# Kernel optimization log

Hardware: AMD Instinct MI355X
Metric: run time of the kernel (lower is better)

Reference implementation:

```python
import jax, jax.numpy as jnp
import numpy as np
import math

S, D, H, L, V = 1024, 768, 12, 6, 32000
KD = D // H
FF = 4 * D
PAD = 0


def setup_inputs() -> dict:
    key = jax.random.key(0)
    ks = jax.random.split(key, 20)
    s = D ** -0.5
    return {
        "token_ids": jax.random.randint(ks[0], (2, S), 0, V, dtype=jnp.int32),
        "emb": jax.random.normal(ks[1], (V, D)) * s,
        "Wq": jax.random.normal(ks[2], (L, H, D, KD)) * s,
        "bq": jnp.zeros((L, H, KD)),
        "Wk": jax.random.normal(ks[3], (L, H, D, KD)) * s,
        "bk": jnp.zeros((L, H, KD)),
        "Wv": jax.random.normal(ks[4], (L, H, D, D)) * s,
        "bv": jnp.zeros((L, H, D)),
        "g1": jnp.ones((L, D)), "be1": jnp.zeros((L, D)),
        "g2": jnp.ones((L, D)), "be2": jnp.zeros((L, D)),
        "W1": jax.random.normal(ks[5], (L, D, FF)) * s,
        "b1": jnp.zeros((L, FF)),
        "W2": jax.random.normal(ks[6], (L, FF, D)) * (FF ** -0.5),
        "b2": jnp.zeros((L, D)),
        "Wout": jax.random.normal(ks[7], (D, V)) * s,
        "bout": jnp.zeros((V,)),
    }


def _pe():
    pos = jnp.arange(S, dtype=jnp.float32)[:, None]
    div = jnp.exp(jnp.arange(0, D, 2, dtype=jnp.float32) * (-math.log(10000.0) / D))
    ang = pos * div  # [S, D/2]
    return jnp.stack([jnp.sin(ang), jnp.cos(ang)], axis=-1).reshape(S, D)


def _ln(x, g, b):
    m = x.mean(-1, keepdims=True)
    v = ((x - m) ** 2).mean(-1, keepdims=True)
    return (x - m) * jax.lax.rsqrt(v + 1e-5) * g + b


def reference(token_ids, emb, Wq, bq, Wk, bk, Wv, bv, g1, be1, g2, be2, W1, b1, W2, b2, Wout, bout):
    pad = token_ids == PAD  # [B,S]
    causal = jnp.triu(jnp.ones((S, S), dtype=bool), k=1)
    # mask[b,s,t] = causal | pad-as-key | pad-as-query
    mask = causal[None, None] | pad[:, None, None, :] | pad[:, None, :, None]  # [B,1,S,S]
    scale = math.sqrt(KD)
    x = emb[token_ids] + _pe()[None]  # [B,S,D]
    for l in range(L):
        q = jnp.einsum('bsd,hdk->bhsk', x, Wq[l]) + bq[l][None, :, None, :]
        k = jnp.einsum('bsd,hdk->bhsk', x, Wk[l]) + bk[l][None, :, None, :]
        v = jnp.einsum('bsd,hde->bhse', x, Wv[l]) + bv[l][None, :, None, :]
        scores = jnp.einsum('bhsk,bhtk->bhst', q, k) / scale
        scores = jnp.where(mask, -jnp.inf, scores)
        all_masked = jnp.all(mask, axis=-1)  # rows with every key masked -> uniform attn
        scores = jnp.where(all_masked[..., None], 0.0, scores)
        attn = jax.nn.softmax(scores, axis=-1)
        heads = jnp.einsum('bhst,bhte->bhse', attn, v)  # per-head full-D values
        attn_out = heads.mean(axis=1)  # heads are AVERAGED, not concatenated
        x = _ln(x + attn_out, g1[l], be1[l])
        ff = jax.nn.relu(x @ W1[l] + b1[l]) @ W2[l] + b2[l]
        x = _ln(x + ff, g2[l], be2[l])
    return x @ Wout + bout
```

## Files before the change

kernel.cpp:

```cpp
#include <hip/hip_runtime.h>
#include <hip/hip_bf16.h>

#define SQ 1024
#define DM 768
#define NH 12
#define NL 6
#define NV 32000
#define KDH 64
#define FFD 3072

using bf16 = __hip_bfloat16;
typedef __attribute__((ext_vector_type(4))) float f32x4;
typedef __attribute__((ext_vector_type(8))) short bf16x8;

__global__ void fill_kernel(float* __restrict__ out, long n, float val) {
  const long stride = (long)gridDim.x * blockDim.x;
  for (long i = (long)blockIdx.x * blockDim.x + threadIdx.x; i < n; i += stride)
    out[i] = val;
}

__device__ __forceinline__ void gload16(const void* g, void* l) {
  __builtin_amdgcn_global_load_lds(
      (const __attribute__((address_space(1))) unsigned int*)g,
      (__attribute__((address_space(3))) unsigned int*)l, 16, 0, 0);
}

template<bool OUT_BF16, bool RELU>
__global__ __launch_bounds__(256) void gemm_bt(
    int M, int N, int K,
    const bf16* __restrict__ Ap, long sAz, int lda,
    const bf16* __restrict__ Bp, long sBz, int ldbt,
    const float* __restrict__ biasp, int sBiasZ,
    void* __restrict__ Cp, long sCz, long sCb, long sCs, long sCn)
{
  __shared__ __align__(16) char lds[32768];
  char* const As = lds;
  char* const Bs = lds + 8192;

  const int tid = threadIdx.x;
  const int gx = gridDim.x, gy = gridDim.y;
  const int nwg = gx * gy * (int)gridDim.z;
  int flat = ((int)blockIdx.z * gy + (int)blockIdx.y) * gx + (int)blockIdx.x;
  {
    const int q = nwg >> 3, r = nwg & 7;
    const int xcd = flat & 7, loc = flat >> 3;
    flat = (xcd < r ? xcd * (q + 1) : r * (q + 1) + (xcd - r) * q) + loc;
  }
  const int bx  = flat % gx;
  const int byz = flat / gx;
  const int m0 = bx * 128;
  const int n0 = (byz % gy) * 128;
  const int z  = byz / gy;

  const int lane = tid & 63;
  const int wid  = tid >> 6;
  const int wm = (wid >> 1) * 64;
  const int wn = (wid & 1) * 64;

  const int srow  = tid >> 2;
  const int sslot = tid & 3;
  const int xorb  = (sslot ^ (srow & 3)) << 4;

  const char* gA0 = (const char*)(Ap + (long)z * sAz + (long)(m0 + srow) * lda) + xorb;
  const char* gA1 = (const char*)(Ap + (long)z * sAz + (long)(m0 + srow + 64) * lda) + xorb;
  const char* gB0 = (const char*)(Bp + (long)z * sBz + (long)(n0 + srow) * ldbt) + xorb;
  const char* gB1 = (const char*)(Bp + (long)z * sBz + (long)(n0 + srow + 64) * ldbt) + xorb;

  auto stage = [&](int dstOfs) {
    gload16(gA0, As + dstOfs + tid * 16);
    gload16(gA1, As + dstOfs + (tid + 256) * 16);
    gload16(gB0, Bs + dstOfs + tid * 16);
    gload16(gB1, Bs + dstOfs + (tid + 256) * 16);
    gA0 += 64; gA1 += 64; gB0 += 64; gB1 += 64;
  };

  const int fr = lane & 15;
  const int kq = lane >> 4;
  const char* fA[4];
  const char* fB[4];
#pragma unroll
  for (int m = 0; m < 4; ++m) {
    const int R = wm + m * 16 + fr;
    fA[m] = As + R * 64 + ((kq ^ (R & 3)) << 4);
  }
#pragma unroll
  for (int n = 0; n < 4; ++n) {
    const int R = wn + n * 16 + fr;
    fB[n] = Bs + R * 64 + ((kq ^ (R & 3)) << 4);
  }

  f32x4 acc[4][4] = {};

  stage(0);
  int cur = 0;
  for (int kt = 0; kt < K; kt += 32) {
    if (kt + 32 < K) {
      stage((cur ^ 1) * 16384);
      asm volatile("s_waitcnt vmcnt(4)" ::: "memory");
    } else {
      asm volatile("s_waitcnt vmcnt(0)" ::: "memory");
    }
    __builtin_amdgcn_s_barrier();
    const int co = cur * 16384;
    bf16x8 af[4], bfr[4];
#pragma unroll
    for (int m = 0; m < 4; ++m) af[m] = *(const bf16x8*)(fA[m] + co);
#pragma unroll
    for (int n = 0; n < 4; ++n) bfr[n] = *(const bf16x8*)(fB[n] + co);
#pragma unroll
    for (int m = 0; m < 4; ++m)
#pragma unroll
      for (int n = 0; n < 4; ++n)
        acc[m][n] = __builtin_amdgcn_mfma_f32_16x16x32_bf16(af[m], bfr[n], acc[m][n], 0, 0, 0);
    __builtin_amdgcn_s_barrier();
    cur ^= 1;
  }

  const int rg = (lane >> 4) * 4;
  const int cl = lane & 15;
#pragma unroll
  for (int n = 0; n < 4; ++n) {
    const int gcol = n0 + wn + n * 16 + cl;
    float bias = 0.f;
    if (biasp) bias = biasp[(long)z * sBiasZ + gcol];
    if (OUT_BF16 && sCs == 1) {
#pragma unroll
      for (int m = 0; m < 4; ++m) {
        const int grow = m0 + wm + m * 16 + rg;
        const long ci = (long)z * sCz + (long)(grow >> 10) * sCb
                      + (long)(grow & 1023) + (long)gcol * sCn;
        ushort4 pk;
        float v0 = acc[m][n][0] + bias, v1 = acc[m][n][1] + bias;
        float v2 = acc[m][n][2] + bias, v3 = acc[m][n][3] + bias;
        if (RELU) { v0 = fmaxf(v0, 0.f); v1 = fmaxf(v1, 0.f);
                    v2 = fmaxf(v2, 0.f); v3 = fmaxf(v3, 0.f); }
        pk.x = __builtin_bit_cast(ushort, __float2bfloat16(v0));
        pk.y = __builtin_bit_cast(ushort, __float2bfloat16(v1));
        pk.z = __builtin_bit_cast(ushort, __float2bfloat16(v2));
        pk.w = __builtin_bit_cast(ushort, __float2bfloat16(v3));
        *(ushort4*)((bf16*)Cp + ci) = pk;
      }
    } else {
#pragma unroll
      for (int m = 0; m < 4; ++m) {
#pragma unroll
        for (int rr = 0; rr < 4; ++rr) {
          const int grow = m0 + wm + m * 16 + rg + rr;
          float v = acc[m][n][rr] + bias;
          if (RELU) v = fmaxf(v, 0.f);
          const long ci = (long)z * sCz + (long)(grow >> 10) * sCb
                        + (long)(grow & 1023) * sCs + (long)gcol * sCn;
          if (OUT_BF16) ((bf16*)Cp)[ci] = __float2bfloat16(v);
          else          ((float*)Cp)[ci] = v;
        }
      }
    }
  }
}

__global__ __launch_bounds__(256) void transpose_kernel(
    const float* __restrict__ in, long sInZ, int ldin,
    bf16* __restrict__ out, long sOutZ, int ldout)
{
  __shared__ float t[64][65];
  const int tid = threadIdx.x;
  const int n0 = blockIdx.x * 64, k0 = blockIdx.y * 64;
  const float* ip = in + (long)blockIdx.z * sInZ;
  bf16* op = out + (long)blockIdx.z * sOutZ;
  const int cx = (tid & 15) * 4, ry = tid >> 4;
#pragma unroll
  for (int p = 0; p < 4; ++p) {
    const int k = ry + p * 16;
    const float4 v = *(const float4*)(ip + (long)(k0 + k) * ldin + n0 + cx);
    t[k][cx] = v.x; t[k][cx + 1] = v.y; t[k][cx + 2] = v.z; t[k][cx + 3] = v.w;
  }
  __syncthreads();
#pragma unroll
  for (int p = 0; p < 4; ++p) {
    const int n = ry + p * 16;
    ushort4 o;
    o.x = __builtin_bit_cast(ushort, __float2bfloat16(t[cx + 0][n]));
    o.y = __builtin_bit_cast(ushort, __float2bfloat16(t[cx + 1][n]));
    o.z = __builtin_bit_cast(ushort, __float2bfloat16(t[cx + 2][n]));
    o.w = __builtin_bit_cast(ushort, __float2bfloat16(t[cx + 3][n]));
    *(ushort4*)(op + (long)(n0 + n) * ldout + k0 + cx) = o;
  }
}

__global__ void biasqk_kernel(const float* __restrict__ bq, const float* __restrict__ bk,
                              float* __restrict__ out) {
  const int i = blockIdx.x * 256 + threadIdx.x;
  if (i < NH * 128) {
    const int h = i >> 7, n = i & 127;
    out[i] = (n < 64) ? bq[h * 64 + n] : bk[h * 64 + n - 64];
  }
}

__global__ __launch_bounds__(256) void embed_kernel(
    const int* __restrict__ tok, const float* __restrict__ emb,
    float* __restrict__ x, bf16* __restrict__ xb)
{
  const int gid = blockIdx.x * 256 + threadIdx.x;
  const int row = gid / (DM / 4);
  const int dc  = (gid % (DM / 4)) * 4;
  const int t = tok[row];
  const int s = row & (SQ - 1);
#pragma unroll
  for (int j = 0; j < 4; ++j) {
    const int d = dc + j;
    const float e = emb[(long)t * DM + d];
    const float div = expf(-(float)(d & ~1) * (9.210340371976184f / (float)DM));
    const float ang = (float)s * div;
    const float pe = (d & 1) ? cosf(ang) : sinf(ang);
    const float v = e + pe;
    x[(long)row * DM + d] = v;
    xb[(long)row * DM + d] = __float2bfloat16(v);
  }
}

__global__ __launch_bounds__(256) void softmax_kernel(
    bf16* __restrict__ P, const int* __restrict__ tok)
{
  const int row = blockIdx.x;
  const int s = row & (SQ - 1);
  const int z = row >> 10;
  const int b = z / NH;
  bf16* sp = P + (long)row * SQ;
  const int* tb = tok + b * SQ;
  const int tid = threadIdx.x;
  const int t0 = tid * 4;

  if (tb[s] == 0) {
    const bf16 u = __float2bfloat16(1.0f / (float)SQ);
    sp[t0] = u; sp[t0 + 1] = u; sp[t0 + 2] = u; sp[t0 + 3] = u;
    return;
  }
  uint2 raw = *(const uint2*)(sp + t0);
  int4 tv = *(const int4*)(tb + t0);
  const bf16* rh = (const bf16*)&raw;
  const int tvv[4] = {tv.x, tv.y, tv.z, tv.w};
  float val[4];
  float vmax = -1e30f;
#pragma unroll
  for (int j = 0; j < 4; ++j) {
    const int t = t0 + j;
    const bool valid = (t <= s) && (tvv[j] != 0);
    val[j] = valid ? __bfloat162float(rh[j]) * 0.125f : -1e30f;
    vmax = fmaxf(vmax, val[j]);
  }
  __shared__ float red[4];
  const int lane = tid & 63, wid = tid >> 6;
  float w = vmax;
#pragma unroll
  for (int o = 32; o >= 1; o >>= 1) w = fmaxf(w, __shfl_xor(w, o));
  if (lane == 0) red[wid] = w;
  __syncthreads();
  const float Mx = fmaxf(fmaxf(red[0], red[1]), fmaxf(red[2], red[3]));
  __syncthreads();
  float e[4]; float lsum = 0.f;
#pragma unroll
  for (int j = 0; j < 4; ++j) {
    e[j] = (val[j] > -1e29f) ? expf(val[j] - Mx) : 0.f;
    lsum += e[j];
  }
  w = lsum;
#pragma unroll
  for (int o = 32; o >= 1; o >>= 1) w += __shfl_xor(w, o);
  if (lane == 0) red[wid] = w;
  __syncthreads();
  const float inv = 1.0f / (red[0] + red[1] + red[2] + red[3]);
#pragma unroll
  for (int j = 0; j < 4; ++j) sp[t0 + j] = __float2bfloat16(e[j] * inv);
}

template<int MODE>
__global__ __launch_bounds__(256) void ln_kernel(
    float* __restrict__ x, bf16* __restrict__ xb,
    const float* __restrict__ tmp, const bf16* __restrict__ heads,
    const float* __restrict__ g, const float* __restrict__ be)
{
  const int r = blockIdx.x;
  const int b = r >> 10;
  const int s = r & (SQ - 1);
  const int tid = threadIdx.x;
  float vals[3];
  float sum = 0.f, sq = 0.f;
#pragma unroll
  for (int i = 0; i < 3; ++i) {
    const int d = tid + i * 256;
    const float a = x[(long)r * DM + d];
    float t;
    if (MODE == 0) {
      t = tmp[(long)r * DM + d];
    } else {
      float hs = 0.f;
#pragma unroll
      for (int h = 0; h < NH; ++h)
        hs += __bfloat162float(heads[((long)(b * NH + h) * SQ + s) * DM + d]);
      t = hs * (1.0f / (float)NH);
    }
    const float vv = a + t;
    vals[i] = vv;
    sum += vv; sq += vv * vv;
  }
  __shared__ float rs[4], rq[4];
  const int lane = tid & 63, wid = tid >> 6;
  float s1 = sum, s2 = sq;
#pragma unroll
  for (int o = 32; o >= 1; o >>= 1) { s1 += __shfl_xor(s1, o); s2 += __shfl_xor(s2, o); }
  if (lane == 0) { rs[wid] = s1; rq[wid] = s2; }
  __syncthreads();
  const float S1 = rs[0] + rs[1] + rs[2] + rs[3];
  const float S2 = rq[0] + rq[1] + rq[2] + rq[3];
  const float mean = S1 * (1.0f / (float)DM);
  const float var  = S2 * (1.0f / (float)DM) - mean * mean;
  const float rstd = rsqrtf(var + 1e-5f);
#pragma unroll
  for (int i = 0; i < 3; ++i) {
    const int d = tid + i * 256;
    const float o = (vals[i] - mean) * rstd * g[d] + be[d];
    x[(long)r * DM + d] = o;
    xb[(long)r * DM + d] = __float2bfloat16(o);
  }
}

extern "C" void kernel_launch(void* const* d_in, const int* in_sizes, int n_in,
                              void* d_out, int out_size, void* d_ws, size_t ws_size,
                              hipStream_t stream) {
  const int expect_sizes[18] = {
    2048, 24576000, 3538944, 4608, 3538944, 4608, 42467328, 55296,
    4608, 4608, 4608, 4608, 14155776, 18432, 14155776, 4608, 24576000, 32000
  };
  bool sizes_ok = (n_in == 18);
  if (sizes_ok)
    for (int i = 0; i < 18; ++i) sizes_ok = sizes_ok && (in_sizes[i] == expect_sizes[i]);
  if (!sizes_ok) {
    fill_kernel<<<2048, 256, 0, stream>>>((float*)d_out, (long)out_size, 1000.0f);
    return;
  }
  if (out_size != 65536000) {
    fill_kernel<<<2048, 256, 0, stream>>>((float*)d_out, (long)out_size, 3000.0f);
    return;
  }
  if (ws_size < 158081024ull) {
    fill_kernel<<<2048, 256, 0, stream>>>((float*)d_out, (long)out_size, 2000.0f);
    return;
  }

  const int*   tok  = (const int*)d_in[0];
  const float* emb  = (const float*)d_in[1];
  const float* Wq   = (const float*)d_in[2];
  const float* bq   = (const float*)d_in[3];
  const float* Wk   = (const float*)d_in[4];
  const float* bk   = (const float*)d_in[5];
  const float* Wv   = (const float*)d_in[6];
  const float* bv   = (const float*)d_in[7];
  const float* g1   = (const float*)d_in[8];
  const float* be1  = (const float*)d_in[9];
  const float* g2   = (const float*)d_in[10];
  const float* be2  = (const float*)d_in[11];
  const float* W1   = (const float*)d_in[12];
  const float* b1   = (const float*)d_in[13];
  const float* W2   = (const float*)d_in[14];
  const float* b2   = (const float*)d_in[15];
  const float* Wout = (const float*)d_in[16];
  const float* bout = (const float*)d_in[17];

  char* ws = (char*)d_ws;
  float* x      = (float*)(ws + 0);
  bf16*  xb     = (bf16*) (ws + 6291456);
  bf16*  qk     = (bf16*) (ws + 9437184);
  float* tmp    = (float*)(ws + 9437184);
  bf16*  vT     = (bf16*) (ws + 15728640);
  bf16*  P      = (bf16*) (ws + 53477376);
  bf16*  ff     = (bf16*) (ws + 53477376);
  bf16*  woutT  = (bf16*) (ws + 53477376);
  bf16*  heads  = (bf16*) (ws + 103809024);
  bf16*  wqkT   = (bf16*) (ws + 141557760);
  bf16*  wvT    = (bf16*) (ws + 143917056);
  bf16*  w1T    = (bf16*) (ws + 141557760);
  bf16*  w2T    = (bf16*) (ws + 146276352);
  float* biasqk = (float*)(ws + 158072832);

  embed_kernel<<<dim3((2 * SQ * DM / 4) / 256), 256, 0, stream>>>(tok, emb, x, xb);

  for (int l = 0; l < NL; ++l) {
    transpose_kernel<<<dim3(1, 12, NH), 256, 0, stream>>>(
        Wq + (long)l * NH * DM * KDH, (long)DM * KDH, KDH,
        wqkT, 128 * DM, DM);
    transpose_kernel<<<dim3(1, 12, NH), 256, 0, stream>>>(
        Wk + (long)l * NH * DM * KDH, (long)DM * KDH, KDH,
        wqkT + 64 * DM, 128 * DM, DM);
    transpose_kernel<<<dim3(12, 12, NH), 256, 0, stream>>>(
        Wv + (long)l * NH * DM * DM, (long)DM * DM, DM,
        wvT, (long)DM * DM, DM);
    biasqk_kernel<<<6, 256, 0, stream>>>(bq + l * NH * KDH, bk + l * NH * KDH, biasqk);

    gemm_bt<true, false><<<dim3(16, 1, NH), 256, 0, stream>>>(
        2048, 128, DM, xb, 0, DM, wqkT, (long)128 * DM, DM,
        biasqk, 128,
        qk, (long)SQ * 128, (long)NH * SQ * 128, 128, 1);
    gemm_bt<true, false><<<dim3(16, 6, NH), 256, 0, stream>>>(
        2048, DM, DM, xb, 0, DM, wvT, (long)DM * DM, DM,
        bv + (long)l * NH * DM, DM,
        vT, (long)DM * SQ, (long)NH * DM * SQ, 1, SQ);
    gemm_bt<true, false><<<dim3(8, 8, 2 * NH), 256, 0, stream>>>(
        SQ, SQ, KDH, qk, (long)SQ * 128, 128, qk + 64, (long)SQ * 128, 128,
        (const float*)nullptr, 0,
        P, (long)SQ * SQ, 0, SQ, 1);
    softmax_kernel<<<dim3(2 * NH * SQ), 256, 0, stream>>>(P, tok);
    gemm_bt<true, false><<<dim3(8, 6, 2 * NH), 256, 0, stream>>>(
        SQ, DM, SQ, P, (long)SQ * SQ, SQ, vT, (long)DM * SQ, SQ,
        (const float*)nullptr, 0,
        heads, (long)SQ * DM, 0, DM, 1);
    ln_kernel<1><<<dim3(2048), 256, 0, stream>>>(x, xb, nullptr, heads,
                                                 g1 + l * DM, be1 + l * DM);
    transpose_kernel<<<dim3(48, 12, 1), 256, 0, stream>>>(
        W1 + (long)l * DM * FFD, 0, FFD, w1T, 0, DM);
    transpose_kernel<<<dim3(12, 48, 1), 256, 0, stream>>>(
        W2 + (long)l * FFD * DM, 0, DM, w2T, 0, FFD);
    gemm_bt<true, true><<<dim3(16, 24, 1), 256, 0, stream>>>(
        2048, FFD, DM, xb, 0, DM, w1T, 0, DM,
        b1 + (long)l * FFD, 0,
        ff, 0, (long)SQ * FFD, FFD, 1);
    gemm_bt<false, false><<<dim3(16, 6, 1), 256, 0, stream>>>(
        2048, DM, FFD, ff, 0, FFD, w2T, 0, FFD,
        b2 + (long)l * DM, 0,
        tmp, 0, (long)SQ * DM, DM, 1);
    ln_kernel<0><<<dim3(2048), 256, 0, stream>>>(x, xb, tmp, nullptr,
                                                 g2 + l * DM, be2 + l * DM);
  }
  transpose_kernel<<<dim3(500, 12, 1), 256, 0, stream>>>(Wout, 0, NV, woutT, 0, DM);
  gemm_bt<false, false><<<dim3(16, 250, 1), 256, 0, stream>>>(
      2048, NV, DM, xb, 0, DM, woutT, 0, DM,
      bout, 0,
      d_out, 0, (long)SQ * NV, NV, 1);
}
```

Baseline: 1.750 ms.

## Exploit causal mask to skip upper-triangle score tiles and truncate PV reduction

Result: no change. 1.769 ms (+1.0%).

```diff
diff --git a/kernel.cpp b/kernel.cpp
--- a/kernel.cpp
+++ b/kernel.cpp
@@ -25,7 +25,7 @@
       (__attribute__((address_space(3))) unsigned int*)l, 16, 0, 0);
 }
 
-template<bool OUT_BF16, bool RELU>
+template<bool OUT_BF16, bool RELU, bool CSKIP = false, bool CTRUNC = false>
 __global__ __launch_bounds__(256) void gemm_bt(
     int M, int N, int K,
     const bf16* __restrict__ Ap, long sAz, int lda,
@@ -52,6 +52,9 @@
   const int n0 = (byz % gy) * 128;
   const int z  = byz / gy;
 
+  if (CSKIP && n0 > m0) return;
+  const int KK = CTRUNC ? min(K, m0 + 128) : K;
+
   const int lane = tid & 63;
   const int wid  = tid >> 6;
   const int wm = (wid >> 1) * 64;
@@ -93,8 +96,8 @@
 
   stage(0);
   int cur = 0;
-  for (int kt = 0; kt < K; kt += 32) {
-    if (kt + 32 < K) {
+  for (int kt = 0; kt < KK; kt += 32) {
+    if (kt + 32 < KK) {
       stage((cur ^ 1) * 16384);
       asm volatile("s_waitcnt vmcnt(4)" ::: "memory");
     } else {
@@ -196,6 +199,58 @@
   }
 }
 
+__global__ __launch_bounds__(256) void xpart_kernel(
+    const float* __restrict__ x, float* __restrict__ xpart) {
+  const int b = blockIdx.x, g = blockIdx.y;
+  const int tid = threadIdx.x;
+  const float* xp = x + (long)b * SQ * DM + (long)g * 64 * DM;
+  float a0 = 0.f, a1 = 0.f, a2 = 0.f;
+  for (int s = 0; s < 64; ++s) {
+    a0 += xp[(long)s * DM + tid];
+    a1 += xp[(long)s * DM + tid + 256];
+    a2 += xp[(long)s * DM + tid + 512];
+  }
+  float* op = xpart + (long)(b * 16 + g) * DM;
+  op[tid] = a0; op[tid + 256] = a1; op[tid + 512] = a2;
+}
+
+__global__ void xmeanf_kernel(const float* __restrict__ xpart, float* __restrict__ xmean) {
+  const int b = blockIdx.x;
+  const int d = threadIdx.x;
+  float a = 0.f;
+#pragma unroll
+  for (int g = 0; g < 16; ++g) a += xpart[(long)(b * 16 + g) * DM + d];
+  xmean[b * DM + d] = a * (1.0f / (float)SQ);
+}
+
+__global__ __launch_bounds__(256) void vmeanw_kernel(
+    const float* __restrict__ xmean, const bf16* __restrict__ wvT,
+    const float* __restrict__ bv, float* __restrict__ vmean) {
+  const int tid = threadIdx.x;
+  const int w = blockIdx.x * 4 + (tid >> 6);
+  const int b = w / DM;
+  const int e = w % DM;
+  const int lane = tid & 63;
+  float xm[12];
+#pragma unroll
+  for (int j = 0; j < 12; ++j) xm[j] = xmean[b * DM + lane + j * 64];
+  float acc = 0.f;
+  for (int h = 0; h < NH; ++h) {
+    const bf16* wr = wvT + ((long)h * DM + e) * DM;
+#pragma unroll
+    for (int j = 0; j < 12; ++j)
+      acc += xm[j] * __bfloat162float(wr[lane + j * 64]);
+  }
+#pragma unroll
+  for (int o = 32; o >= 1; o >>= 1) acc += __shfl_xor(acc, o);
+  if (lane == 0) {
+    float bs = 0.f;
+#pragma unroll
+    for (int h = 0; h < NH; ++h) bs += bv[h * DM + e];
+    vmean[b * DM + e] = (acc + bs) * (1.0f / (float)NH);
+  }
+}
+
 __global__ __launch_bounds__(256) void embed_kernel(
     const int* __restrict__ tok, const float* __restrict__ emb,
     float* __restrict__ x, bf16* __restrict__ xb)
@@ -277,12 +332,13 @@
 __global__ __launch_bounds__(256) void ln_kernel(
     float* __restrict__ x, bf16* __restrict__ xb,
     const float* __restrict__ tmp, const bf16* __restrict__ heads,
-    const float* __restrict__ g, const float* __restrict__ be)
+    const float* __restrict__ g, const float* __restrict__ be,
+    const int* __restrict__ tok, const float* __restrict__ vmean)
 {
   const int r = blockIdx.x;
   const int b = r >> 10;
-  const int s = r & (SQ - 1);
   const int tid = threadIdx.x;
+  const bool pad = (MODE == 1) && (tok[r] == 0);
   float vals[3];
   float sum = 0.f, sq = 0.f;
 #pragma unroll
@@ -292,7 +348,10 @@
     float t;
     if (MODE == 0) {
       t = tmp[(long)r * DM + d];
+    } else if (pad) {
+      t = vmean[b * DM + d];
     } else {
+      const int s = r & (SQ - 1);
       float hs = 0.f;
 #pragma unroll
       for (int h = 0; h < NH; ++h)
@@ -342,7 +401,7 @@
     fill_kernel<<<2048, 256, 0, stream>>>((float*)d_out, (long)out_size, 3000.0f);
     return;
   }
-  if (ws_size < 158081024ull) {
+  if (ws_size < 158189568ull) {
     fill_kernel<<<2048, 256, 0, stream>>>((float*)d_out, (long)out_size, 2000.0f);
     return;
   }
@@ -381,6 +440,9 @@
   bf16*  w1T    = (bf16*) (ws + 141557760);
   bf16*  w2T    = (bf16*) (ws + 146276352);
   float* biasqk = (float*)(ws + 158072832);
+  float* xpart  = (float*)(ws + 158078976);
+  float* xmean  = (float*)(ws + 158177280);
+  float* vmean  = (float*)(ws + 158183424);
 
   embed_kernel<<<dim3((2 * SQ * DM / 4) / 256), 256, 0, stream>>>(tok, emb, x, xb);
 
@@ -396,6 +458,10 @@
         wvT, (long)DM * DM, DM);
     biasqk_kernel<<<6, 256, 0, stream>>>(bq + l * NH * KDH, bk + l * NH * KDH, biasqk);
 
+    xpart_kernel<<<dim3(2, 16), 256, 0, stream>>>(x, xpart);
+    xmeanf_kernel<<<dim3(2), 768, 0, stream>>>(xpart, xmean);
+    vmeanw_kernel<<<dim3(384), 256, 0, stream>>>(xmean, wvT, bv + (long)l * NH * DM, vmean);
+
     gemm_bt<true, false><<<dim3(16, 1, NH), 256, 0, stream>>>(
         2048, 128, DM, xb, 0, DM, wqkT, (long)128 * DM, DM,
         biasqk, 128,
@@ -404,17 +470,17 @@
         2048, DM, DM, xb, 0, DM, wvT, (long)DM * DM, DM,
         bv + (long)l * NH * DM, DM,
         vT, (long)DM * SQ, (long)NH * DM * SQ, 1, SQ);
-    gemm_bt<true, false><<<dim3(8, 8, 2 * NH), 256, 0, stream>>>(
+    gemm_bt<true, false, true, false><<<dim3(8, 8, 2 * NH), 256, 0, stream>>>(
         SQ, SQ, KDH, qk, (long)SQ * 128, 128, qk + 64, (long)SQ * 128, 128,
         (const float*)nullptr, 0,
         P, (long)SQ * SQ, 0, SQ, 1);
     softmax_kernel<<<dim3(2 * NH * SQ), 256, 0, stream>>>(P, tok);
-    gemm_bt<true, false><<<dim3(8, 6, 2 * NH), 256, 0, stream>>>(
+    gemm_bt<true, false, false, true><<<dim3(8, 6, 2 * NH), 256, 0, stream>>>(
         SQ, DM, SQ, P, (long)SQ * SQ, SQ, vT, (long)DM * SQ, SQ,
         (const float*)nullptr, 0,
         heads, (long)SQ * DM, 0, DM, 1);
     ln_kernel<1><<<dim3(2048), 256, 0, stream>>>(x, xb, nullptr, heads,
-                                                 g1 + l * DM, be1 + l * DM);
+                                                 g1 + l * DM, be1 + l * DM, tok, vmean);
     transpose_kernel<<<dim3(48, 12, 1), 256, 0, stream>>>(
         W1 + (long)l * DM * FFD, 0, FFD, w1T, 0, DM);
     transpose_kernel<<<dim3(12, 48, 1), 256, 0, stream>>>(
@@ -428,7 +494,7 @@
         b2 + (long)l * DM, 0,
         tmp, 0, (long)SQ * DM, DM, 1);
     ln_kernel<0><<<dim3(2048), 256, 0, stream>>>(x, xb, tmp, nullptr,
-                                                 g2 + l * DM, be2 + l * DM);
+                                                 g2 + l * DM, be2 + l * DM, tok, nullptr);
   }
   transpose_kernel<<<dim3(500, 12, 1), 256, 0, stream>>>(Wout, 0, NV, woutT, 0, DM);
   gemm_bt<false, false><<<dim3(16, 250, 1), 256, 0, stream>>>(
```
